# Kernel optimization log

Hardware: AMD Instinct MI355X
Metric: run time of the kernel (lower is better)

## Reference

```python
import jax, jax.numpy as jnp
import numpy as np

D_MODEL = 1024
H = 16
D_K = D_MODEL // H  # 64


def setup_inputs() -> dict:
    key = jax.random.key(0)
    ks = jax.random.split(key, 10)
    B, S = 4, 4096
    q = jax.random.normal(ks[0], (B, S, D_MODEL), dtype=jnp.float32)
    k = jax.random.normal(ks[1], (B, S, D_MODEL), dtype=jnp.float32)
    v = jax.random.normal(ks[2], (B, S, D_MODEL), dtype=jnp.float32)
    m = jax.random.uniform(ks[3], (B, S), dtype=jnp.float32)
    sc = 1.0 / np.sqrt(D_MODEL)
    Wq = jax.random.uniform(ks[4], (D_MODEL, D_K), jnp.float32, -sc, sc)
    bq = jax.random.uniform(ks[5], (D_K,), jnp.float32, -sc, sc)
    Wk = jax.random.uniform(ks[6], (D_MODEL, D_K), jnp.float32, -sc, sc)
    bk = jax.random.uniform(ks[7], (D_K,), jnp.float32, -sc, sc)
    Wv = jax.random.uniform(ks[8], (D_MODEL, D_K), jnp.float32, -sc, sc)
    bv = jax.random.uniform(ks[9], (D_K,), jnp.float32, -sc, sc)
    return {"q": q, "k": k, "v": v, "m": m,
            "Wq": Wq, "bq": bq, "Wk": Wk, "bk": bk, "Wv": Wv, "bv": bv}


def reference(q, k, v, m, Wq, bq, Wk, bk, Wv, bv):
    # single-head projections: [B,S,d_model] -> [B,S,d_k]
    qh = q @ Wq + bq
    kh = k @ Wk + bk
    vh = v @ Wv + bv
    # scaled dot-product scores [B,S,S]
    a = jnp.einsum("bqd,bkd->bqk", qh, kh) / jnp.sqrt(jnp.float32(D_K))
    # multiplicative per-query-row mask BEFORE softmax (non-standard variant)
    a = a * m[:, :, None]
    a = jax.nn.softmax(a, axis=-1)
    # AV: [B,S,S] x [B,S,d_k] -> [B,S,d_k]
    y = jnp.einsum("bqk,bkd->bqd", a, vh)
    return y
```

## Files before the change

### kernel.cpp

```cpp
#include <hip/hip_runtime.h>


typedef __attribute__((ext_vector_type(8))) short short8;
typedef __attribute__((ext_vector_type(4))) float float4v;
typedef __attribute__((ext_vector_type(4))) unsigned int uint4v;

#define DEV static __device__ __forceinline__

DEV unsigned short f2bf(float f) {
  unsigned int x; __builtin_memcpy(&x, &f, 4);
  x += 0x7fff + ((x >> 16) & 1);
  return (unsigned short)(x >> 16);
}
DEV void stage8(unsigned short* dst, const float* src) {
  float4v a = *(const float4v*)src;
  float4v b = *(const float4v*)(src + 4);
  unsigned short tmp[8];
#pragma unroll
  for (int i = 0; i < 4; ++i) { tmp[i] = f2bf(a[i]); tmp[4 + i] = f2bf(b[i]); }
  __builtin_memcpy(dst, tmp, 16);
}

__global__ __launch_bounds__(256) void transpose_w(
    const float* __restrict__ Wq, const float* __restrict__ Wk,
    const float* __restrict__ Wv, unsigned short* __restrict__ WT) {
  int idx = blockIdx.x * 256 + threadIdx.x;
  int p = idx >> 16;
  int r = idx & 65535;
  int kk = r >> 6, d = r & 63;
  const float* W = (p == 0) ? Wq : (p == 1) ? Wk : Wv;
  WT[p * 65536 + d * 1024 + kk] = f2bf(W[r]);
}

__global__ __launch_bounds__(256) void proj_kernel(
    const float* __restrict__ xq, const float* __restrict__ xk,
    const float* __restrict__ xv, const float* __restrict__ mmask,
    const float* __restrict__ bq, const float* __restrict__ bk,
    const float* __restrict__ bv, const unsigned short* __restrict__ WT,
    unsigned short* __restrict__ qs, unsigned short* __restrict__ khh,
    unsigned short* __restrict__ vhT) {
  constexpr int LDSTR = 88;
  __shared__ __align__(16) unsigned short Xs[64 * LDSTR];
  __shared__ __align__(16) unsigned short Ws[64 * LDSTR];

  const int p = blockIdx.x >> 8;
  const int rt = blockIdx.x & 255;
  const int row0 = rt * 64;
  const int t = threadIdx.x;
  const int w = t >> 6, ln = t & 63;
  const int lr = ln & 15, quad = ln >> 4;

  const float* X = (p == 0) ? xq : (p == 1) ? xk : xv;
  const unsigned short* WTp = WT + p * 65536;

  float4v acc[4];
#pragma unroll
  for (int i = 0; i < 4; ++i) acc[i] = (float4v){0.f, 0.f, 0.f, 0.f};

  const int srow = t >> 3;
  const int scol = (t & 7) * 8;

  for (int kc = 0; kc < 16; ++kc) {
    const int k0 = kc * 64;
#pragma unroll
    for (int pass = 0; pass < 2; ++pass) {
      int rr = srow + pass * 32;
      stage8(&Xs[rr * LDSTR + scol], &X[(size_t)(row0 + rr) * 1024 + k0 + scol]);
      *(uint4v*)&Ws[rr * LDSTR + scol] =
          *(const uint4v*)&WTp[(size_t)rr * 1024 + k0 + scol];
    }
    __syncthreads();
    if (p < 2) {
#pragma unroll
      for (int ks = 0; ks < 2; ++ks) {
        short8 af = *(const short8*)&Xs[(w * 16 + lr) * LDSTR + ks * 32 + quad * 8];
#pragma unroll
        for (int ct = 0; ct < 4; ++ct) {
          short8 bf = *(const short8*)&Ws[(ct * 16 + lr) * LDSTR + ks * 32 + quad * 8];
          acc[ct] = __builtin_amdgcn_mfma_f32_16x16x32_bf16(af, bf, acc[ct], 0, 0, 0);
        }
      }
    } else {
#pragma unroll
      for (int ks = 0; ks < 2; ++ks) {
        short8 af = *(const short8*)&Ws[(w * 16 + lr) * LDSTR + ks * 32 + quad * 8];
#pragma unroll
        for (int ct = 0; ct < 4; ++ct) {
          short8 bf = *(const short8*)&Xs[(ct * 16 + lr) * LDSTR + ks * 32 + quad * 8];
          acc[ct] = __builtin_amdgcn_mfma_f32_16x16x32_bf16(af, bf, acc[ct], 0, 0, 0);
        }
      }
    }
    __syncthreads();
  }

  if (p == 0) {
    const float L2E8 = 1.4426950408889634f * 0.125f;
#pragma unroll
    for (int r = 0; r < 4; ++r) {
      int sg = row0 + w * 16 + quad * 4 + r;
      float mv = mmask[sg] * L2E8;
#pragma unroll
      for (int ct = 0; ct < 4; ++ct) {
        int d = ct * 16 + lr;
        qs[(size_t)sg * 64 + d] = f2bf((acc[ct][r] + bq[d]) * mv);
      }
    }
  } else if (p == 1) {
#pragma unroll
    for (int r = 0; r < 4; ++r) {
      int sg = row0 + w * 16 + quad * 4 + r;
#pragma unroll
      for (int ct = 0; ct < 4; ++ct) {
        int d = ct * 16 + lr;
        khh[(size_t)sg * 64 + d] = f2bf(acc[ct][r] + bk[d]);
      }
    }
  } else {
    int b = row0 >> 12, sloc = row0 & 4095;
#pragma unroll
    for (int r = 0; r < 4; ++r) {
      int d = w * 16 + quad * 4 + r;
      float bias = bv[d];
#pragma unroll
      for (int ct = 0; ct < 4; ++ct) {
        int sg = sloc + ct * 16 + lr;
        vhT[(size_t)b * 64 * 4096 + (size_t)d * 4096 + sg] = f2bf(acc[ct][r] + bias);
      }
    }
  }
}

#define SPLITS 4
__global__ __launch_bounds__(256) void attn_split(
    const unsigned short* __restrict__ qs, const unsigned short* __restrict__ khh,
    const unsigned short* __restrict__ vhT, float* __restrict__ O_part,
    float* __restrict__ L_part) {
  constexpr int LDSTR = 88;
  __shared__ __align__(16) unsigned short Ks[64 * LDSTR];
  __shared__ __align__(16) unsigned short Vs[64 * LDSTR];
  __shared__ __align__(16) unsigned short Ps[4 * 16 * LDSTR];

  const int split = blockIdx.x >> 8;
  const int rest  = blockIdx.x & 255;
  const int b = rest >> 6;
  const int s0 = (rest & 63) * 64;
  const int t = threadIdx.x, w = t >> 6, ln = t & 63;
  const int lr = ln & 15, quad = ln >> 4;

  const size_t qrow = (size_t)(b * 4096 + s0 + w * 16 + lr) * 64;
  short8 qf0 = *(const short8*)&qs[qrow + quad * 8];
  short8 qf1 = *(const short8*)&qs[qrow + 32 + quad * 8];

  float Lacc[4] = {0.f, 0.f, 0.f, 0.f};
  float4v O[4];
#pragma unroll
  for (int i = 0; i < 4; ++i) O[i] = (float4v){0.f, 0.f, 0.f, 0.f};

  const int srow = t >> 3, scol = (t & 7) * 8;
  const unsigned short* Kg = khh + (size_t)b * 4096 * 64;
  const unsigned short* Vg = vhT + (size_t)b * 64 * 4096;
  unsigned short* Pw = Ps + w * 16 * LDSTR;

  for (int kt = 0; kt < 16; ++kt) {
    const int k0 = split * 1024 + kt * 64;
#pragma unroll
    for (int pass = 0; pass < 2; ++pass) {
      int rr = srow + pass * 32;
      *(uint4v*)&Ks[rr * LDSTR + scol] =
          *(const uint4v*)&Kg[(size_t)(k0 + rr) * 64 + scol];
      *(uint4v*)&Vs[rr * LDSTR + scol] =
          *(const uint4v*)&Vg[(size_t)rr * 4096 + k0 + scol];
    }
    __syncthreads();

    float4v sc[4];
#pragma unroll
    for (int ct = 0; ct < 4; ++ct) {
      sc[ct] = (float4v){0.f, 0.f, 0.f, 0.f};
      short8 kf0 = *(const short8*)&Ks[(ct * 16 + lr) * LDSTR + quad * 8];
      short8 kf1 = *(const short8*)&Ks[(ct * 16 + lr) * LDSTR + 32 + quad * 8];
      sc[ct] = __builtin_amdgcn_mfma_f32_16x16x32_bf16(qf0, kf0, sc[ct], 0, 0, 0);
      sc[ct] = __builtin_amdgcn_mfma_f32_16x16x32_bf16(qf1, kf1, sc[ct], 0, 0, 0);
    }

#pragma unroll
    for (int ct = 0; ct < 4; ++ct)
#pragma unroll
      for (int r = 0; r < 4; ++r) {
        float pv = exp2f(sc[ct][r]);
        sc[ct][r] = pv;
        Lacc[r] += pv;
        Pw[(quad * 4 + r) * LDSTR + ct * 16 + lr] = f2bf(pv);
      }

    __asm__ volatile("s_waitcnt lgkmcnt(0)" ::: "memory");

    short8 pf0 = *(const short8*)&Pw[lr * LDSTR + quad * 8];
    short8 pf1 = *(const short8*)&Pw[lr * LDSTR + 32 + quad * 8];
#pragma unroll
    for (int dt = 0; dt < 4; ++dt) {
      short8 vf0 = *(const short8*)&Vs[(dt * 16 + lr) * LDSTR + quad * 8];
      short8 vf1 = *(const short8*)&Vs[(dt * 16 + lr) * LDSTR + 32 + quad * 8];
      O[dt] = __builtin_amdgcn_mfma_f32_16x16x32_bf16(pf0, vf0, O[dt], 0, 0, 0);
      O[dt] = __builtin_amdgcn_mfma_f32_16x16x32_bf16(pf1, vf1, O[dt], 0, 0, 0);
    }
    __syncthreads();
  }

#pragma unroll
  for (int r = 0; r < 4; ++r) {
    float s = Lacc[r];
    s += __shfl_xor(s, 1);
    s += __shfl_xor(s, 2);
    s += __shfl_xor(s, 4);
    s += __shfl_xor(s, 8);
    Lacc[r] = s;
  }

#pragma unroll
  for (int r = 0; r < 4; ++r) {
    int prow = b * 4096 + s0 + w * 16 + quad * 4 + r;
    size_t obase = ((size_t)split * 16384 + prow) * 64;
#pragma unroll
    for (int dt = 0; dt < 4; ++dt)
      O_part[obase + dt * 16 + lr] = O[dt][r];
    if (lr == 0) L_part[(size_t)split * 16384 + prow] = Lacc[r];
  }
}

__global__ __launch_bounds__(256) void attn_reduce(
    const float* __restrict__ O_part, const float* __restrict__ L_part,
    float* __restrict__ out) {
  size_t idx = (size_t)blockIdx.x * 256 + threadIdx.x;
  size_t row = idx >> 6;
  float l = L_part[row] + L_part[16384 + row] + L_part[2 * 16384 + row] +
            L_part[3 * 16384 + row];
  float o = O_part[idx] + O_part[idx + (size_t)16384 * 64] +
            O_part[idx + (size_t)2 * 16384 * 64] +
            O_part[idx + (size_t)3 * 16384 * 64];
  out[idx] = o / l;
}

extern "C" void kernel_launch(void* const* d_in, const int* in_sizes, int n_in,
                              void* d_out, int out_size, void* d_ws, size_t ws_size,
                              hipStream_t stream) {
  const float* q  = (const float*)d_in[0];
  const float* k  = (const float*)d_in[1];
  const float* v  = (const float*)d_in[2];
  const float* m  = (const float*)d_in[3];
  const float* Wq = (const float*)d_in[4];
  const float* bq = (const float*)d_in[5];
  const float* Wk = (const float*)d_in[6];
  const float* bk = (const float*)d_in[7];
  const float* Wv = (const float*)d_in[8];
  const float* bv = (const float*)d_in[9];
  float* out = (float*)d_out;

  unsigned short* ws16 = (unsigned short*)d_ws;
  unsigned short* WT  = ws16;
  unsigned short* qs  = WT + 3 * 65536;
  unsigned short* kh  = qs + 16384 * 64;
  unsigned short* vhT = kh + 16384 * 64;
  float* O_part = (float*)(vhT + 16384 * 64);
  float* L_part = O_part + (size_t)SPLITS * 16384 * 64;

  transpose_w<<<dim3(768), dim3(256), 0, stream>>>(Wq, Wk, Wv, WT);
  proj_kernel<<<dim3(768), dim3(256), 0, stream>>>(q, k, v, m, bq, bk, bv, WT,
                                                   qs, kh, vhT);
  attn_split<<<dim3(SPLITS * 256), dim3(256), 0, stream>>>(qs, kh, vhT,
                                                           O_part, L_part);
  attn_reduce<<<dim3(4096), dim3(256), 0, stream>>>(O_part, L_part, out);
}
```

Before: 263.9 us.

## Register-prefetch next tiles in projection and attention kernels, widen projection K-chunk

```diff
diff --git a/kernel.cpp b/kernel.cpp
--- a/kernel.cpp
+++ b/kernel.cpp
@@ -11,14 +11,6 @@
   unsigned int x; __builtin_memcpy(&x, &f, 4);
   x += 0x7fff + ((x >> 16) & 1);
   return (unsigned short)(x >> 16);
-}
-DEV void stage8(unsigned short* dst, const float* src) {
-  float4v a = *(const float4v*)src;
-  float4v b = *(const float4v*)(src + 4);
-  unsigned short tmp[8];
-#pragma unroll
-  for (int i = 0; i < 4; ++i) { tmp[i] = f2bf(a[i]); tmp[4 + i] = f2bf(b[i]); }
-  __builtin_memcpy(dst, tmp, 16);
 }
 
 __global__ __launch_bounds__(256) void transpose_w(
@@ -39,7 +31,7 @@
     const float* __restrict__ bv, const unsigned short* __restrict__ WT,
     unsigned short* __restrict__ qs, unsigned short* __restrict__ khh,
     unsigned short* __restrict__ vhT) {
-  constexpr int LDSTR = 88;
+  constexpr int LDSTR = 136;
   __shared__ __align__(16) unsigned short Xs[64 * LDSTR];
   __shared__ __align__(16) unsigned short Ws[64 * LDSTR];
 
@@ -52,27 +44,50 @@
 
   const float* X = (p == 0) ? xq : (p == 1) ? xk : xv;
   const unsigned short* WTp = WT + p * 65536;
+  const float* Xbase = X + (size_t)row0 * 1024;
 
   float4v acc[4];
 #pragma unroll
   for (int i = 0; i < 4; ++i) acc[i] = (float4v){0.f, 0.f, 0.f, 0.f};
 
-  const int srow = t >> 3;
-  const int scol = (t & 7) * 8;
-
-  for (int kc = 0; kc < 16; ++kc) {
-    const int k0 = kc * 64;
-#pragma unroll
-    for (int pass = 0; pass < 2; ++pass) {
-      int rr = srow + pass * 32;
-      stage8(&Xs[rr * LDSTR + scol], &X[(size_t)(row0 + rr) * 1024 + k0 + scol]);
-      *(uint4v*)&Ws[rr * LDSTR + scol] =
-          *(const uint4v*)&WTp[(size_t)rr * 1024 + k0 + scol];
+  const int srow = t >> 4;
+  const int scol = (t & 15) * 8;
+
+  float4v xr[4][2];
+  uint4v wr[4];
+
+#define ISSUE(kc_)                                                         \
+  {                                                                        \
+    const int k0_ = (kc_) * 128;                                           \
+    _Pragma("unroll") for (int ps = 0; ps < 4; ++ps) {                     \
+      const int rr = srow + ps * 16;                                       \
+      const float* s_ = Xbase + (size_t)rr * 1024 + k0_ + scol;            \
+      xr[ps][0] = *(const float4v*)s_;                                     \
+      xr[ps][1] = *(const float4v*)(s_ + 4);                               \
+      wr[ps] = *(const uint4v*)&WTp[(size_t)rr * 1024 + k0_ + scol];       \
+    }                                                                      \
+  }
+
+  ISSUE(0);
+  for (int kc = 0; kc < 8; ++kc) {
+#pragma unroll
+    for (int ps = 0; ps < 4; ++ps) {
+      const int rr = srow + ps * 16;
+      unsigned short tmp[8];
+#pragma unroll
+      for (int i = 0; i < 4; ++i) {
+        tmp[i] = f2bf(xr[ps][0][i]);
+        tmp[4 + i] = f2bf(xr[ps][1][i]);
+      }
+      __builtin_memcpy(&Xs[rr * LDSTR + scol], tmp, 16);
+      *(uint4v*)&Ws[rr * LDSTR + scol] = wr[ps];
     }
     __syncthreads();
+    if (kc < 7) ISSUE(kc + 1);
+
     if (p < 2) {
 #pragma unroll
-      for (int ks = 0; ks < 2; ++ks) {
+      for (int ks = 0; ks < 4; ++ks) {
         short8 af = *(const short8*)&Xs[(w * 16 + lr) * LDSTR + ks * 32 + quad * 8];
 #pragma unroll
         for (int ct = 0; ct < 4; ++ct) {
@@ -82,7 +97,7 @@
       }
     } else {
 #pragma unroll
-      for (int ks = 0; ks < 2; ++ks) {
+      for (int ks = 0; ks < 4; ++ks) {
         short8 af = *(const short8*)&Ws[(w * 16 + lr) * LDSTR + ks * 32 + quad * 8];
 #pragma unroll
         for (int ct = 0; ct < 4; ++ct) {
@@ -93,6 +108,7 @@
     }
     __syncthreads();
   }
+#undef ISSUE
 
   if (p == 0) {
     const float L2E8 = 1.4426950408889634f * 0.125f;
@@ -162,17 +178,28 @@
   const unsigned short* Vg = vhT + (size_t)b * 64 * 4096;
   unsigned short* Pw = Ps + w * 16 * LDSTR;
 
+  uint4v kr[2], vr[2];
+
+#define ISSUE_KV(kt_)                                                       \
+  {                                                                         \
+    const int k0_ = split * 1024 + (kt_) * 64;                              \
+    _Pragma("unroll") for (int ps = 0; ps < 2; ++ps) {                      \
+      const int rr = srow + ps * 32;                                        \
+      kr[ps] = *(const uint4v*)&Kg[(size_t)(k0_ + rr) * 64 + scol];         \
+      vr[ps] = *(const uint4v*)&Vg[(size_t)rr * 4096 + k0_ + scol];         \
+    }                                                                       \
+  }
+
+  ISSUE_KV(0);
   for (int kt = 0; kt < 16; ++kt) {
-    const int k0 = split * 1024 + kt * 64;
-#pragma unroll
-    for (int pass = 0; pass < 2; ++pass) {
-      int rr = srow + pass * 32;
-      *(uint4v*)&Ks[rr * LDSTR + scol] =
-          *(const uint4v*)&Kg[(size_t)(k0 + rr) * 64 + scol];
-      *(uint4v*)&Vs[rr * LDSTR + scol] =
-          *(const uint4v*)&Vg[(size_t)rr * 4096 + k0 + scol];
+#pragma unroll
+    for (int ps = 0; ps < 2; ++ps) {
+      const int rr = srow + ps * 32;
+      *(uint4v*)&Ks[rr * LDSTR + scol] = kr[ps];
+      *(uint4v*)&Vs[rr * LDSTR + scol] = vr[ps];
     }
     __syncthreads();
+    if (kt < 15) ISSUE_KV(kt + 1);
 
     float4v sc[4];
 #pragma unroll
@@ -189,7 +216,6 @@
 #pragma unroll
       for (int r = 0; r < 4; ++r) {
         float pv = exp2f(sc[ct][r]);
-        sc[ct][r] = pv;
         Lacc[r] += pv;
         Pw[(quad * 4 + r) * LDSTR + ct * 16 + lr] = f2bf(pv);
       }
@@ -207,6 +233,7 @@
     }
     __syncthreads();
   }
+#undef ISSUE_KV
 
 #pragma unroll
   for (int r = 0; r < 4; ++r) {
```

Result: no change. 261.6 us (-0.9%).

## Double-buffer projection loads and read K/V fragments directly in attention with more splits

Applied to the files above, without the earlier changes.

```diff
diff --git a/kernel.cpp b/kernel.cpp
--- a/kernel.cpp
+++ b/kernel.cpp
@@ -12,13 +12,9 @@
   x += 0x7fff + ((x >> 16) & 1);
   return (unsigned short)(x >> 16);
 }
-DEV void stage8(unsigned short* dst, const float* src) {
-  float4v a = *(const float4v*)src;
-  float4v b = *(const float4v*)(src + 4);
-  unsigned short tmp[8];
-#pragma unroll
-  for (int i = 0; i < 4; ++i) { tmp[i] = f2bf(a[i]); tmp[4 + i] = f2bf(b[i]); }
-  __builtin_memcpy(dst, tmp, 16);
+
+DEV void lds_barrier() {
+  __asm__ volatile("s_waitcnt lgkmcnt(0)\n\ts_barrier" ::: "memory");
 }
 
 __global__ __launch_bounds__(256) void transpose_w(
@@ -39,9 +35,9 @@
     const float* __restrict__ bv, const unsigned short* __restrict__ WT,
     unsigned short* __restrict__ qs, unsigned short* __restrict__ khh,
     unsigned short* __restrict__ vhT) {
-  constexpr int LDSTR = 88;
-  __shared__ __align__(16) unsigned short Xs[64 * LDSTR];
-  __shared__ __align__(16) unsigned short Ws[64 * LDSTR];
+  constexpr int LDSTR = 72;
+  __shared__ __align__(16) unsigned short Xs[2][64 * LDSTR];
+  __shared__ __align__(16) unsigned short Ws[2][64 * LDSTR];
 
   const int p = blockIdx.x >> 8;
   const int rt = blockIdx.x & 255;
@@ -52,47 +48,72 @@
 
   const float* X = (p == 0) ? xq : (p == 1) ? xk : xv;
   const unsigned short* WTp = WT + p * 65536;
+  const float* Xbase = X + (size_t)row0 * 1024;
 
   float4v acc[4];
 #pragma unroll
   for (int i = 0; i < 4; ++i) acc[i] = (float4v){0.f, 0.f, 0.f, 0.f};
 
-  const int srow = t >> 3;
-  const int scol = (t & 7) * 8;
-
+  const int srow = t >> 2;
+  const int scol = (t & 3) * 16;
+
+  float4v xr[2][4];
+  uint4v wr[2][2];
+
+#define PISSUE(kc_, b_)                                                    \
+  {                                                                        \
+    const int c0_ = (kc_) * 64 + scol;                                     \
+    const float* xs_ = Xbase + (size_t)srow * 1024 + c0_;                  \
+    xr[b_][0] = *(const float4v*)xs_;                                      \
+    xr[b_][1] = *(const float4v*)(xs_ + 4);                                \
+    xr[b_][2] = *(const float4v*)(xs_ + 8);                                \
+    xr[b_][3] = *(const float4v*)(xs_ + 12);                               \
+    const unsigned short* wsp_ = WTp + (size_t)srow * 1024 + c0_;          \
+    wr[b_][0] = *(const uint4v*)wsp_;                                      \
+    wr[b_][1] = *(const uint4v*)(wsp_ + 8);                                \
+  }
+
+  PISSUE(0, 0);
+#pragma unroll
   for (int kc = 0; kc < 16; ++kc) {
-    const int k0 = kc * 64;
-#pragma unroll
-    for (int pass = 0; pass < 2; ++pass) {
-      int rr = srow + pass * 32;
-      stage8(&Xs[rr * LDSTR + scol], &X[(size_t)(row0 + rr) * 1024 + k0 + scol]);
-      *(uint4v*)&Ws[rr * LDSTR + scol] =
-          *(const uint4v*)&WTp[(size_t)rr * 1024 + k0 + scol];
-    }
-    __syncthreads();
+    const int b = kc & 1;
+    if (kc < 15) PISSUE(kc + 1, b ^ 1);
+
+    unsigned short tmp[16];
+#pragma unroll
+    for (int i = 0; i < 4; ++i)
+#pragma unroll
+      for (int j = 0; j < 4; ++j) tmp[i * 4 + j] = f2bf(xr[b][i][j]);
+    *(uint4v*)&Xs[b][srow * LDSTR + scol] = *(const uint4v*)&tmp[0];
+    *(uint4v*)&Xs[b][srow * LDSTR + scol + 8] = *(const uint4v*)&tmp[8];
+    *(uint4v*)&Ws[b][srow * LDSTR + scol] = wr[b][0];
+    *(uint4v*)&Ws[b][srow * LDSTR + scol + 8] = wr[b][1];
+
+    lds_barrier();
+
     if (p < 2) {
 #pragma unroll
       for (int ks = 0; ks < 2; ++ks) {
-        short8 af = *(const short8*)&Xs[(w * 16 + lr) * LDSTR + ks * 32 + quad * 8];
+        short8 af = *(const short8*)&Xs[b][(w * 16 + lr) * LDSTR + ks * 32 + quad * 8];
 #pragma unroll
         for (int ct = 0; ct < 4; ++ct) {
-          short8 bf = *(const short8*)&Ws[(ct * 16 + lr) * LDSTR + ks * 32 + quad * 8];
+          short8 bf = *(const short8*)&Ws[b][(ct * 16 + lr) * LDSTR + ks * 32 + quad * 8];
           acc[ct] = __builtin_amdgcn_mfma_f32_16x16x32_bf16(af, bf, acc[ct], 0, 0, 0);
         }
       }
     } else {
 #pragma unroll
       for (int ks = 0; ks < 2; ++ks) {
-        short8 af = *(const short8*)&Ws[(w * 16 + lr) * LDSTR + ks * 32 + quad * 8];
+        short8 af = *(const short8*)&Ws[b][(w * 16 + lr) * LDSTR + ks * 32 + quad * 8];
 #pragma unroll
         for (int ct = 0; ct < 4; ++ct) {
-          short8 bf = *(const short8*)&Xs[(ct * 16 + lr) * LDSTR + ks * 32 + quad * 8];
+          short8 bf = *(const short8*)&Xs[b][(ct * 16 + lr) * LDSTR + ks * 32 + quad * 8];
           acc[ct] = __builtin_amdgcn_mfma_f32_16x16x32_bf16(af, bf, acc[ct], 0, 0, 0);
         }
       }
     }
-    __syncthreads();
-  }
+  }
+#undef PISSUE
 
   if (p == 0) {
     const float L2E8 = 1.4426950408889634f * 0.125f;
@@ -131,14 +152,11 @@
   }
 }
 
-#define SPLITS 4
 __global__ __launch_bounds__(256) void attn_split(
     const unsigned short* __restrict__ qs, const unsigned short* __restrict__ khh,
     const unsigned short* __restrict__ vhT, float* __restrict__ O_part,
-    float* __restrict__ L_part) {
-  constexpr int LDSTR = 88;
-  __shared__ __align__(16) unsigned short Ks[64 * LDSTR];
-  __shared__ __align__(16) unsigned short Vs[64 * LDSTR];
+    float* __restrict__ L_part, int nkt) {
+  constexpr int LDSTR = 72;
   __shared__ __align__(16) unsigned short Ps[4 * 16 * LDSTR];
 
   const int split = blockIdx.x >> 8;
@@ -147,6 +165,7 @@
   const int s0 = (rest & 63) * 64;
   const int t = threadIdx.x, w = t >> 6, ln = t & 63;
   const int lr = ln & 15, quad = ln >> 4;
+  const int key0 = split * nkt * 64;
 
   const size_t qrow = (size_t)(b * 4096 + s0 + w * 16 + lr) * 64;
   short8 qf0 = *(const short8*)&qs[qrow + quad * 8];
@@ -157,29 +176,20 @@
 #pragma unroll
   for (int i = 0; i < 4; ++i) O[i] = (float4v){0.f, 0.f, 0.f, 0.f};
 
-  const int srow = t >> 3, scol = (t & 7) * 8;
   const unsigned short* Kg = khh + (size_t)b * 4096 * 64;
   const unsigned short* Vg = vhT + (size_t)b * 64 * 4096;
   unsigned short* Pw = Ps + w * 16 * LDSTR;
 
-  for (int kt = 0; kt < 16; ++kt) {
-    const int k0 = split * 1024 + kt * 64;
-#pragma unroll
-    for (int pass = 0; pass < 2; ++pass) {
-      int rr = srow + pass * 32;
-      *(uint4v*)&Ks[rr * LDSTR + scol] =
-          *(const uint4v*)&Kg[(size_t)(k0 + rr) * 64 + scol];
-      *(uint4v*)&Vs[rr * LDSTR + scol] =
-          *(const uint4v*)&Vg[(size_t)rr * 4096 + k0 + scol];
-    }
-    __syncthreads();
+  for (int kt = 0; kt < nkt; ++kt) {
+    const int k0 = key0 + kt * 64;
 
     float4v sc[4];
 #pragma unroll
     for (int ct = 0; ct < 4; ++ct) {
+      const unsigned short* kr = &Kg[(size_t)(k0 + ct * 16 + lr) * 64 + quad * 8];
+      short8 kf0 = *(const short8*)kr;
+      short8 kf1 = *(const short8*)(kr + 32);
       sc[ct] = (float4v){0.f, 0.f, 0.f, 0.f};
-      short8 kf0 = *(const short8*)&Ks[(ct * 16 + lr) * LDSTR + quad * 8];
-      short8 kf1 = *(const short8*)&Ks[(ct * 16 + lr) * LDSTR + 32 + quad * 8];
       sc[ct] = __builtin_amdgcn_mfma_f32_16x16x32_bf16(qf0, kf0, sc[ct], 0, 0, 0);
       sc[ct] = __builtin_amdgcn_mfma_f32_16x16x32_bf16(qf1, kf1, sc[ct], 0, 0, 0);
     }
@@ -189,23 +199,21 @@
 #pragma unroll
       for (int r = 0; r < 4; ++r) {
         float pv = exp2f(sc[ct][r]);
-        sc[ct][r] = pv;
         Lacc[r] += pv;
         Pw[(quad * 4 + r) * LDSTR + ct * 16 + lr] = f2bf(pv);
       }
-
     __asm__ volatile("s_waitcnt lgkmcnt(0)" ::: "memory");
 
     short8 pf0 = *(const short8*)&Pw[lr * LDSTR + quad * 8];
     short8 pf1 = *(const short8*)&Pw[lr * LDSTR + 32 + quad * 8];
 #pragma unroll
     for (int dt = 0; dt < 4; ++dt) {
-      short8 vf0 = *(const short8*)&Vs[(dt * 16 + lr) * LDSTR + quad * 8];
-      short8 vf1 = *(const short8*)&Vs[(dt * 16 + lr) * LDSTR + 32 + quad * 8];
+      const unsigned short* vr = &Vg[(size_t)(dt * 16 + lr) * 4096 + k0 + quad * 8];
+      short8 vf0 = *(const short8*)vr;
+      short8 vf1 = *(const short8*)(vr + 32);
       O[dt] = __builtin_amdgcn_mfma_f32_16x16x32_bf16(pf0, vf0, O[dt], 0, 0, 0);
       O[dt] = __builtin_amdgcn_mfma_f32_16x16x32_bf16(pf1, vf1, O[dt], 0, 0, 0);
     }
-    __syncthreads();
   }
 
 #pragma unroll
@@ -231,14 +239,14 @@
 
 __global__ __launch_bounds__(256) void attn_reduce(
     const float* __restrict__ O_part, const float* __restrict__ L_part,
-    float* __restrict__ out) {
+    float* __restrict__ out, int splits) {
   size_t idx = (size_t)blockIdx.x * 256 + threadIdx.x;
   size_t row = idx >> 6;
-  float l = L_part[row] + L_part[16384 + row] + L_part[2 * 16384 + row] +
-            L_part[3 * 16384 + row];
-  float o = O_part[idx] + O_part[idx + (size_t)16384 * 64] +
-            O_part[idx + (size_t)2 * 16384 * 64] +
-            O_part[idx + (size_t)3 * 16384 * 64];
+  float l = 0.f, o = 0.f;
+  for (int s = 0; s < splits; ++s) {
+    l += L_part[(size_t)s * 16384 + row];
+    o += O_part[idx + (size_t)s * 16384 * 64];
+  }
   out[idx] = o / l;
 }
 
@@ -263,12 +271,17 @@
   unsigned short* kh  = qs + 16384 * 64;
   unsigned short* vhT = kh + 16384 * 64;
   float* O_part = (float*)(vhT + 16384 * 64);
-  float* L_part = O_part + (size_t)SPLITS * 16384 * 64;
+
+  const size_t base_bytes = (size_t)(3 * 65536 + 3 * 16384 * 64) * 2;
+  int splits = 8;
+  if (ws_size < base_bytes + (size_t)8 * 16384 * 65 * 4) splits = 4;
+  float* L_part = O_part + (size_t)splits * 16384 * 64;
+  const int nkt = 64 / splits;
 
   transpose_w<<<dim3(768), dim3(256), 0, stream>>>(Wq, Wk, Wv, WT);
   proj_kernel<<<dim3(768), dim3(256), 0, stream>>>(q, k, v, m, bq, bk, bv, WT,
                                                    qs, kh, vhT);
-  attn_split<<<dim3(SPLITS * 256), dim3(256), 0, stream>>>(qs, kh, vhT,
-                                                           O_part, L_part);
-  attn_reduce<<<dim3(4096), dim3(256), 0, stream>>>(O_part, L_part, out);
-}
+  attn_split<<<dim3(splits * 256), dim3(256), 0, stream>>>(qs, kh, vhT,
+                                                           O_part, L_part, nkt);
+  attn_reduce<<<dim3(4096), dim3(256), 0, stream>>>(O_part, L_part, out, splits);
+}
```

New measurement: 348.0 us. +31.9%, slower.
